# Performance work log

Measured on AMD Instinct MI355X. Metric: run time of the kernel, lower is better.

The kernel has to match this reference:

```python
import jax, jax.numpy as jnp
import numpy as np
import math

B, S, H, D = 2, 2048, 12, 768


def setup_inputs() -> dict:
    key = jax.random.key(0)
    ks = jax.random.split(key, 7)
    std = 0.02
    x = jax.random.normal(ks[0], (B, S, D), jnp.float32)
    W_q = std * jax.random.normal(ks[1], (H, D, D), jnp.float32)
    W_k = std * jax.random.normal(ks[2], (H, D, D), jnp.float32)
    W_v = std * jax.random.normal(ks[3], (H, D, D), jnp.float32)
    W_o = (std / math.sqrt(2 * 12)) * jax.random.normal(ks[4], (D, H * D), jnp.float32)
    ff_w1 = std * jax.random.normal(ks[5], (4 * D, D), jnp.float32)
    ff_w2 = std * jax.random.normal(ks[6], (D, 4 * D), jnp.float32)
    return {"x": x, "W_q": W_q, "W_k": W_k, "W_v": W_v, "W_o": W_o,
            "ff_w1": ff_w1, "ff_w2": ff_w2}


def _layernorm(x, eps=1e-5):
    # LayerNorm(elementwise_affine=False)
    mu = jnp.mean(x, axis=-1, keepdims=True)
    var = jnp.var(x, axis=-1, keepdims=True)
    return (x - mu) * jax.lax.rsqrt(var + eps)


def reference(x, W_q, W_k, W_v, W_o, ff_w1, ff_w2):
    b, s, d = x.shape
    h = W_q.shape[0]
    # per-head FULL-width projections: x is shared across heads
    Q = jnp.einsum('bsd,hde->bhse', x, W_q)
    K = jnp.einsum('bsd,hde->bhse', x, W_k)
    V = jnp.einsum('bsd,hde->bhse', x, W_v)
    scores = jnp.einsum('bhqe,bhke->bhqk', Q, K) / math.sqrt(d)  # [B,H,S,S]
    causal = jnp.tril(jnp.ones((s, s), dtype=bool))
    scores = jnp.where(causal[None, None], scores, jnp.finfo(scores.dtype).min)
    attn = jax.nn.softmax(scores, axis=-1)
    ctx = jnp.einsum('bhqk,bhke->bhqe', attn, V)            # [B,H,S,D]
    ctx = ctx.transpose(0, 2, 1, 3).reshape(b, s, h * d)     # [B,S,H*D]
    out = ctx @ W_o.T                                        # [B,S,D]
    # FFN: LN(no affine) -> Linear(d,4d) -> GELU(exact) -> Linear(4d,d); dropout=eval no-op
    hdn = jax.nn.gelu(_layernorm(out) @ ff_w1.T, approximate=False)
    out = out + hdn @ ff_w2.T
    return out
```

## Files before the change

kernel.cpp:

```cpp
#include <hip/hip_runtime.h>
#include <math.h>

#define S_   2048
#define D_   768
#define HD_  9216
#define FF_  3072

typedef float  f32x4  __attribute__((ext_vector_type(4)));
typedef __bf16 bf16x8 __attribute__((ext_vector_type(8)));

__device__ __forceinline__ ushort f2bf(float v) {
    return __builtin_bit_cast(ushort, (__bf16)v);
}

__device__ __forceinline__ void load_lds16(const ushort* g, ushort* l) {
    __builtin_amdgcn_global_load_lds(
        (const __attribute__((address_space(1))) void*)g,
        (__attribute__((address_space(3))) void*)l, 16, 0, 0);
}

__device__ __forceinline__ void zero_acc(f32x4 acc[4][4]) {
#pragma unroll
    for (int i = 0; i < 4; ++i)
#pragma unroll
        for (int j = 0; j < 4; ++j) acc[i][j] = (f32x4){0.f, 0.f, 0.f, 0.f};
}

__device__ __forceinline__ void gemm128(
    const ushort* __restrict__ A, int lda,
    const ushort* __restrict__ Bt, int ldb,
    int m0, int n0, int kmax, f32x4 acc[4][4])
{
    __shared__ __align__(16) ushort As[2][128 * 32];
    __shared__ __align__(16) ushort Bs[2][128 * 32];
    const int tid  = threadIdx.x;
    const int lane = tid & 63, wave = tid >> 6;
    const int l16  = lane & 15, quad = lane >> 4;
    const int wr = wave >> 1, wc = wave & 1;
    const int srow = lane >> 2;
    const int scol = (lane & 3) << 3;

    const ushort* Ab = A + (size_t)m0 * lda;
    const ushort* Bb = Bt + (size_t)n0 * ldb;

    auto stage = [&](int k0, int buf) {
#pragma unroll
        for (int c = 0; c < 2; ++c) {
            const int rb = c * 64 + wave * 16;
            load_lds16(Ab + (size_t)(rb + srow) * lda + k0 + scol,
                       &As[buf][rb * 32]);
            load_lds16(Bb + (size_t)(rb + srow) * ldb + k0 + scol,
                       &Bs[buf][rb * 32]);
        }
    };

    stage(0, 0);
    __syncthreads();
    int cur = 0;
    for (int k0 = 0; k0 < kmax; k0 += 32) {
        if (k0 + 32 < kmax) stage(k0 + 32, cur ^ 1);
        bf16x8 a[4], b[4];
#pragma unroll
        for (int i = 0; i < 4; ++i)
            a[i] = *(const bf16x8*)&As[cur][(wr * 64 + i * 16 + l16) * 32 + quad * 8];
#pragma unroll
        for (int j = 0; j < 4; ++j)
            b[j] = *(const bf16x8*)&Bs[cur][(wc * 64 + j * 16 + l16) * 32 + quad * 8];
#pragma unroll
        for (int i = 0; i < 4; ++i)
#pragma unroll
            for (int j = 0; j < 4; ++j)
                acc[i][j] = __builtin_amdgcn_mfma_f32_16x16x32_bf16(
                    a[i], b[j], acc[i][j], 0, 0, 0);
        __syncthreads();
        cur ^= 1;
    }
}

__device__ __forceinline__ void gemm128_bA(
    const ushort* __restrict__ Ab,
    const ushort* __restrict__ Bt, int ldb,
    int n0, int kmax, f32x4 acc[4][4])
{
    __shared__ __align__(16) ushort As[2][128 * 32];
    __shared__ __align__(16) ushort Bs[2][128 * 32];
    const int tid  = threadIdx.x;
    const int lane = tid & 63, wave = tid >> 6;
    const int l16  = lane & 15, quad = lane >> 4;
    const int wr = wave >> 1, wc = wave & 1;
    const int srow = lane >> 2;
    const int scol = (lane & 3) << 3;

    const ushort* Bb = Bt + (size_t)n0 * ldb;

    auto stage = [&](int k0, int buf) {
        const ushort* At = Ab + (size_t)(k0 >> 7) * 16384 + (k0 & 127);
#pragma unroll
        for (int c = 0; c < 2; ++c) {
            const int rb = c * 64 + wave * 16;
            load_lds16(At + (size_t)(rb + srow) * 128 + scol, &As[buf][rb * 32]);
            load_lds16(Bb + (size_t)(rb + srow) * ldb + k0 + scol,
                       &Bs[buf][rb * 32]);
        }
    };

    stage(0, 0);
    __syncthreads();
    int cur = 0;
    for (int k0 = 0; k0 < kmax; k0 += 32) {
        if (k0 + 32 < kmax) stage(k0 + 32, cur ^ 1);
        bf16x8 a[4], b[4];
#pragma unroll
        for (int i = 0; i < 4; ++i)
            a[i] = *(const bf16x8*)&As[cur][(wr * 64 + i * 16 + l16) * 32 + quad * 8];
#pragma unroll
        for (int j = 0; j < 4; ++j)
            b[j] = *(const bf16x8*)&Bs[cur][(wc * 64 + j * 16 + l16) * 32 + quad * 8];
#pragma unroll
        for (int i = 0; i < 4; ++i)
#pragma unroll
            for (int j = 0; j < 4; ++j)
                acc[i][j] = __builtin_amdgcn_mfma_f32_16x16x32_bf16(
                    a[i], b[j], acc[i][j], 0, 0, 0);
        __syncthreads();
        cur ^= 1;
    }
}

#define EPI_DECL \
    const int lane_ = threadIdx.x & 63, wave_ = threadIdx.x >> 6;   \
    const int l16_ = lane_ & 15, quad_ = lane_ >> 4;                \
    const int wr_ = wave_ >> 1, wc_ = wave_ & 1;
#define RR_ (wr_ * 64 + i * 16 + quad_ * 4 + r)
#define NC_ (wc_ * 64 + j * 16 + l16_)

__global__ __launch_bounds__(256) void convert_kernel(
    const float* __restrict__ in, ushort* __restrict__ out, long n)
{
    long i = ((long)blockIdx.x * 256 + threadIdx.x) * 4;
    const long stride = (long)gridDim.x * 1024;
    for (; i < n; i += stride) {
        float4 v = *(const float4*)&in[i];
        out[i + 0] = f2bf(v.x); out[i + 1] = f2bf(v.y);
        out[i + 2] = f2bf(v.z); out[i + 3] = f2bf(v.w);
    }
}

__global__ __launch_bounds__(256, 2) void gemmNT_kernel(
    const ushort* __restrict__ A, int lda, long aStr,
    const ushort* __restrict__ Bt, int ldb, long bStr,
    ushort* __restrict__ C, int ldc, long cStr, int kmax)
{
    const int z = blockIdx.z;
    const int m0 = blockIdx.y * 128, n0 = blockIdx.x * 128;
    f32x4 acc[4][4];
    zero_acc(acc);
    gemm128(A + (size_t)z * aStr, lda, Bt + (size_t)z * bStr, ldb,
            m0, n0, kmax, acc);
    ushort* out = C + (size_t)z * cStr;
    EPI_DECL
#pragma unroll
    for (int i = 0; i < 4; ++i)
#pragma unroll
        for (int j = 0; j < 4; ++j)
#pragma unroll
            for (int r = 0; r < 4; ++r)
                out[(size_t)(m0 + RR_) * ldc + n0 + NC_] = f2bf(acc[i][j][r]);
}

__global__ __launch_bounds__(256, 2) void xmy_kernel(
    const ushort* __restrict__ Xb, const ushort* __restrict__ MtP,
    const ushort* __restrict__ UtP, ushort* __restrict__ XMp,
    ushort* __restrict__ Yt)
{
    const int z = blockIdx.z;
    const int h = z & 1;
    const bool ymode = z >= 2;
    const int m0 = blockIdx.y * 128, n0 = blockIdx.x * 128;
    const ushort* Bt = (ymode ? UtP : MtP) + (size_t)h * 589824;
    f32x4 acc[4][4];
    zero_acc(acc);
    gemm128(Xb, D_, Bt, D_, m0, n0, D_, acc);
    EPI_DECL
    if (!ymode) {
        ushort* out = XMp + (size_t)h * 3145728;
#pragma unroll
        for (int i = 0; i < 4; ++i)
#pragma unroll
            for (int j = 0; j < 4; ++j)
#pragma unroll
                for (int r = 0; r < 4; ++r)
                    out[(size_t)(m0 + RR_) * D_ + n0 + NC_] = f2bf(acc[i][j][r]);
    } else {
        const int b = m0 >> 11;
        ushort* out = Yt + (size_t)h * 3145728 + (size_t)b * 1572864;
#pragma unroll
        for (int i = 0; i < 4; ++i)
#pragma unroll
            for (int j = 0; j < 4; ++j) {
                ushort4 o4;
                o4.x = f2bf(acc[i][j][0]); o4.y = f2bf(acc[i][j][1]);
                o4.z = f2bf(acc[i][j][2]); o4.w = f2bf(acc[i][j][3]);
                const int nc = n0 + wc_ * 64 + j * 16 + l16_;
                const int s  = (m0 & 2047) + wr_ * 64 + i * 16 + quad_ * 4;
                *(ushort4*)&out[(size_t)nc * 2048 + s] = o4;
            }
    }
}

__global__ __launch_bounds__(256, 2) void scores_c_kernel(
    const ushort* __restrict__ XM, const ushort* __restrict__ Xb,
    ushort* __restrict__ Sc)
{
    const int t = blockIdx.x, b = blockIdx.y, hp = blockIdx.z;
    int mi = (int)((sqrtf(8.f * t + 1.f) - 1.f) * 0.5f);
    while ((mi + 1) * (mi + 2) / 2 <= t) ++mi;
    while (mi * (mi + 1) / 2 > t) --mi;
    const int ni = t - mi * (mi + 1) / 2;
    f32x4 acc[4][4];
    zero_acc(acc);
    gemm128(XM + (size_t)hp * 3145728 + (size_t)b * 1572864, D_,
            Xb + (size_t)b * 1572864, D_, mi * 128, ni * 128, D_, acc);
    ushort* out = Sc + ((size_t)(hp * 2 + b) * 136 + t) * 16384;
    EPI_DECL
#pragma unroll
    for (int i = 0; i < 4; ++i)
#pragma unroll
        for (int j = 0; j < 4; ++j)
#pragma unroll
            for (int r = 0; r < 4; ++r)
                out[(size_t)RR_ * 128 + NC_] = f2bf(acc[i][j][r]);
}

__global__ __launch_bounds__(256) void softmax_c_kernel(ushort* __restrict__ Sc)
{
    const int bx = blockIdx.x;
    const int hp = bx >> 12, b = (bx >> 11) & 1, q = bx & 2047;
    ushort* base = Sc + (size_t)((hp * 2 + b) * 136) * 16384;
    const int mi = q >> 7, tri = mi * (mi + 1) / 2;
    const int L  = (mi + 1) << 7;
    const int ro = (q & 127) << 7;
    const float scale = 0.03608439182435161f;
    const int tid = threadIdx.x;
    const int wave = tid >> 6, lane = tid & 63;

    float xv[8];
    float m = -1e30f;
#pragma unroll
    for (int i = 0; i < 2; ++i) {
        const int k = tid * 4 + i * 1024;
        ushort4 v = {0, 0, 0, 0};
        if (k <= q)
            v = *(const ushort4*)&base[(size_t)(tri + (k >> 7)) * 16384
                                       + ro + (k & 127)];
        xv[i * 4 + 0] = (k + 0 <= q) ? (float)*(__bf16*)&v.x * scale : -1e30f;
        xv[i * 4 + 1] = (k + 1 <= q) ? (float)*(__bf16*)&v.y * scale : -1e30f;
        xv[i * 4 + 2] = (k + 2 <= q) ? (float)*(__bf16*)&v.z * scale : -1e30f;
        xv[i * 4 + 3] = (k + 3 <= q) ? (float)*(__bf16*)&v.w * scale : -1e30f;
#pragma unroll
        for (int j = 0; j < 4; ++j) m = fmaxf(m, xv[i * 4 + j]);
    }
    for (int o = 32; o > 0; o >>= 1) m = fmaxf(m, __shfl_xor(m, o));
    __shared__ float redm[4];
    if (lane == 0) redm[wave] = m;
    __syncthreads();
    m = fmaxf(fmaxf(redm[0], redm[1]), fmaxf(redm[2], redm[3]));

    float e[8];
    float s = 0.f;
#pragma unroll
    for (int i = 0; i < 2; ++i) {
        const int k = tid * 4 + i * 1024;
#pragma unroll
        for (int j = 0; j < 4; ++j) {
            e[i * 4 + j] = (k + j <= q) ? __expf(xv[i * 4 + j] - m) : 0.f;
            s += e[i * 4 + j];
        }
    }
    for (int o = 32; o > 0; o >>= 1) s += __shfl_xor(s, o);
    __shared__ float reds[4];
    if (lane == 0) reds[wave] = s;
    __syncthreads();
    s = reds[0] + reds[1] + reds[2] + reds[3];
    const float inv = 1.f / s;
#pragma unroll
    for (int i = 0; i < 2; ++i) {
        const int k = tid * 4 + i * 1024;
        if (k < L) {
            ushort4 o4;
            o4.x = f2bf(e[i * 4 + 0] * inv);
            o4.y = f2bf(e[i * 4 + 1] * inv);
            o4.z = f2bf(e[i * 4 + 2] * inv);
            o4.w = f2bf(e[i * 4 + 3] * inv);
            *(ushort4*)&base[(size_t)(tri + (k >> 7)) * 16384
                             + ro + (k & 127)] = o4;
        }
    }
}

__global__ __launch_bounds__(256, 2) void py_kernel(
    const ushort* __restrict__ Sc, const ushort* __restrict__ Yt,
    float* __restrict__ AttnA, float* __restrict__ AttnB)
{
    const int z = blockIdx.z;
    const int h = z >> 1, b = z & 1;
    const int mi = 15 - blockIdx.y;
    const int n0 = blockIdx.x * 128;
    const ushort* Ab =
        Sc + ((size_t)(h * 2 + b) * 136 + mi * (mi + 1) / 2) * 16384;
    const ushort* Bt = Yt + (size_t)h * 3145728 + (size_t)b * 1572864;
    f32x4 acc[4][4];
    zero_acc(acc);
    gemm128_bA(Ab, Bt, S_, n0, (mi + 1) << 7, acc);
    float* out = (h ? AttnB : AttnA) + (size_t)b * 1572864
               + (size_t)mi * 128 * D_;
    EPI_DECL
#pragma unroll
    for (int i = 0; i < 4; ++i)
#pragma unroll
        for (int j = 0; j < 4; ++j)
#pragma unroll
            for (int r = 0; r < 4; ++r)
                out[(size_t)RR_ * D_ + n0 + NC_] += acc[i][j][r];
}

__global__ __launch_bounds__(256) void ln_kernel(
    const float* __restrict__ AttnA, const float* __restrict__ AttnB,
    ushort* __restrict__ Ln)
{
    const int row = blockIdx.x;
    const float* a = AttnA + (size_t)row * D_;
    const float* b = AttnB + (size_t)row * D_;
    const int tid = threadIdx.x;
    const int wave = tid >> 6, lane = tid & 63;
    float v0 = a[tid]       + b[tid];
    float v1 = a[tid + 256] + b[tid + 256];
    float v2 = a[tid + 512] + b[tid + 512];
    float s  = v0 + v1 + v2;
    float sq = v0 * v0 + v1 * v1 + v2 * v2;
    for (int o = 32; o > 0; o >>= 1) { s += __shfl_xor(s, o); sq += __shfl_xor(sq, o); }
    __shared__ float rs[4], rq[4];
    if (lane == 0) { rs[wave] = s; rq[wave] = sq; }
    __syncthreads();
    s  = rs[0] + rs[1] + rs[2] + rs[3];
    sq = rq[0] + rq[1] + rq[2] + rq[3];
    const float mean = s * (1.f / 768.f);
    float var = sq * (1.f / 768.f) - mean * mean;
    var = fmaxf(var, 0.f);
    const float rstd = rsqrtf(var + 1e-5f);
    ushort* o = Ln + (size_t)row * D_;
    o[tid]       = f2bf((v0 - mean) * rstd);
    o[tid + 256] = f2bf((v1 - mean) * rstd);
    o[tid + 512] = f2bf((v2 - mean) * rstd);
}

__global__ __launch_bounds__(256, 2) void ffn1_kernel(
    const ushort* __restrict__ Ln, const ushort* __restrict__ F1b,
    ushort* __restrict__ H1)
{
    const int m0 = blockIdx.y * 128, n0 = blockIdx.x * 128;
    f32x4 acc[4][4];
    zero_acc(acc);
    gemm128(Ln, D_, F1b, D_, m0, n0, D_, acc);
    EPI_DECL
#pragma unroll
    for (int i = 0; i < 4; ++i)
#pragma unroll
        for (int j = 0; j < 4; ++j)
#pragma unroll
            for (int r = 0; r < 4; ++r) {
                float v = acc[i][j][r];
                float gl = 0.5f * v * (1.f + erff(v * 0.70710678118654752f));
                H1[(size_t)(m0 + RR_) * FF_ + n0 + NC_] = f2bf(gl);
            }
}

__global__ __launch_bounds__(256, 2) void ffn2p_kernel(
    const ushort* __restrict__ H1, const ushort* __restrict__ F2b,
    float* __restrict__ P2)
{
    const int z = blockIdx.z;
    const int m0 = blockIdx.y * 128, n0 = blockIdx.x * 128;
    f32x4 acc[4][4];
    zero_acc(acc);
    gemm128(H1 + (size_t)z * 1536, FF_, F2b + (size_t)z * 1536, FF_,
            m0, n0, 1536, acc);
    float* out = P2 + (size_t)z * 3145728;
    EPI_DECL
#pragma unroll
    for (int i = 0; i < 4; ++i)
#pragma unroll
        for (int j = 0; j < 4; ++j)
#pragma unroll
            for (int r = 0; r < 4; ++r)
                out[(size_t)(m0 + RR_) * D_ + n0 + NC_] = acc[i][j][r];
}

__global__ __launch_bounds__(256) void ffn2r_kernel(
    const float* __restrict__ P2, const float* __restrict__ AttnA,
    float* __restrict__ Out)
{
    const long i = ((long)blockIdx.x * 256 + threadIdx.x) * 4;
    float4 a = *(const float4*)&P2[i];
    float4 b = *(const float4*)&P2[3145728 + i];
    float4 c = *(const float4*)&AttnA[i];
    float4 d = *(const float4*)&Out[i];
    float4 o;
    o.x = a.x + b.x + c.x + d.x; o.y = a.y + b.y + c.y + d.y;
    o.z = a.z + b.z + c.z + d.z; o.w = a.w + b.w + c.w + d.w;
    *(float4*)&Out[i] = o;
}

extern "C" void kernel_launch(void* const* d_in, const int* in_sizes, int n_in,
                              void* d_out, int out_size, void* d_ws, size_t ws_size,
                              hipStream_t stream)
{
    int ix = -1, iw[4], nw = 0, iff[2], nf = 0;
    for (int i = 0; i < 7; ++i) {
        long sz = in_sizes[i];
        if (sz == 3145728L) ix = i;
        else if (sz == 2359296L) { if (nf < 2) iff[nf++] = i; }
        else { if (nw < 4) iw[nw++] = i; }
    }
    if (ix < 0 || nw != 4 || nf != 2) {
        ix = 0; iw[0] = 1; iw[1] = 2; iw[2] = 3; iw[3] = 4; iff[0] = 5; iff[1] = 6;
    }
    const float* x; const float *Wq, *Wk, *Wv, *Wo, *F1, *F2;
    x  = (const float*)d_in[ix];
    F1 = (const float*)d_in[iff[0]];
    F2 = (const float*)d_in[iff[1]];
    if (ix == 0) {
        Wq = (const float*)d_in[iw[0]]; Wk = (const float*)d_in[iw[1]];
        Wv = (const float*)d_in[iw[2]]; Wo = (const float*)d_in[iw[3]];
    } else {
        Wk = (const float*)d_in[iw[0]]; Wo = (const float*)d_in[iw[1]];
        Wq = (const float*)d_in[iw[2]]; Wv = (const float*)d_in[iw[3]];
    }

    char* p = (char*)d_ws;
    ushort* Xb    = (ushort*)(p + 0);
    ushort* Mt    = (ushort*)(p + 6291456);
    ushort* Ut    = (ushort*)(p + 20447232);
    float*  AttnA = (float*) (p + 34603008);
    ushort* XMp   = (ushort*)(p + 47185920);
    ushort* Yt    = (ushort*)(p + 59768832);
    ushort* Scp   = (ushort*)(p + 72351744);
    float*  AttnB = (float*)d_out;
    ushort* Wa    = (ushort*)(p + 47185920);
    ushort* Wb    = (ushort*)(p + 61341696);
    ushort* H1    = (ushort*)(p + 0);
    ushort* F1b   = (ushort*)(p + 47185920);
    ushort* F2b   = (ushort*)(p + 51904512);
    ushort* Ln    = (ushort*)(p + 56623104);
    float*  P2    = (float*) (p + 62914560);

    dim3 blk(256);
    hipMemsetAsync(AttnA, 0, 12582912, stream);
    hipMemsetAsync(AttnB, 0, 12582912, stream);

    convert_kernel<<<dim3(1024), blk, 0, stream>>>(x, Xb, 3145728L);

    convert_kernel<<<dim3(1024), blk, 0, stream>>>(Wq, Wa, 7077888L);
    convert_kernel<<<dim3(1024), blk, 0, stream>>>(Wk, Wb, 7077888L);
    gemmNT_kernel<<<dim3(6, 6, 12), blk, 0, stream>>>(
        Wb, 768, 589824L, Wa, 768, 589824L, Mt, 768, 589824L, 768);
    convert_kernel<<<dim3(1024), blk, 0, stream>>>(Wv, Wa, 7077888L);
    convert_kernel<<<dim3(1024), blk, 0, stream>>>(Wo, Wb, 7077888L);
    gemmNT_kernel<<<dim3(6, 6, 12), blk, 0, stream>>>(
        Wb, HD_, 768L, Wa, 768, 589824L, Ut, 768, 589824L, 768);

    for (int pr = 0; pr < 6; ++pr) {
        xmy_kernel<<<dim3(6, 32, 4), blk, 0, stream>>>(
            Xb, Mt + (size_t)pr * 1179648, Ut + (size_t)pr * 1179648,
            XMp, Yt);
        scores_c_kernel<<<dim3(136, 2, 2), blk, 0, stream>>>(XMp, Xb, Scp);
        softmax_c_kernel<<<dim3(8192), blk, 0, stream>>>(Scp);
        py_kernel<<<dim3(6, 16, 4), blk, 0, stream>>>(Scp, Yt, AttnA, AttnB);
    }

    convert_kernel<<<dim3(1024), blk, 0, stream>>>(F1, F1b, 2359296L);
    convert_kernel<<<dim3(1024), blk, 0, stream>>>(F2, F2b, 2359296L);
    ln_kernel<<<dim3(4096), blk, 0, stream>>>(AttnA, AttnB, Ln);
    ffn1_kernel<<<dim3(24, 32), blk, 0, stream>>>(Ln, F1b, H1);
    ffn2p_kernel<<<dim3(6, 32, 2), blk, 0, stream>>>(H1, F2b, P2);
    ffn2r_kernel<<<dim3(3072), blk, 0, stream>>>(P2, AttnA, (float*)d_out);
}
```

Before: 1.028 ms.

## Swizzle LDS tiles and prefetch two stages ahead with explicit vmcnt waits

Applies an XOR swizzle to the column chunk used when staging A/B tiles into LDS and when reading them for MFMA, to reduce LDS bank conflicts. Reworks the double-buffered k-loop so the load for step k+64 is issued after compute, with a partial vmcnt wait that keeps one stage of global-to-LDS loads in flight, replacing full __syncthreads waits. This risks ordering bugs if the vmcnt counts are wrong, and adds an extra barrier per iteration.

```diff
diff --git a/kernel.cpp b/kernel.cpp
--- a/kernel.cpp
+++ b/kernel.cpp
@@ -38,7 +38,7 @@
     const int l16  = lane & 15, quad = lane >> 4;
     const int wr = wave >> 1, wc = wave & 1;
     const int srow = lane >> 2;
-    const int scol = (lane & 3) << 3;
+    const int scol = ((lane & 3) ^ ((srow >> 1) & 3)) << 3;
 
     const ushort* Ab = A + (size_t)m0 * lda;
     const ushort* Bb = Bt + (size_t)n0 * ldb;
@@ -55,24 +55,42 @@
     };
 
     stage(0, 0);
-    __syncthreads();
+    if (kmax > 32) {
+        stage(32, 1);
+        asm volatile("s_waitcnt vmcnt(4)" ::: "memory");
+    } else {
+        asm volatile("s_waitcnt vmcnt(0)" ::: "memory");
+    }
+    __builtin_amdgcn_sched_barrier(0);
+    __builtin_amdgcn_s_barrier();
+
+    const int csw = (quad ^ ((l16 >> 1) & 3)) << 3;
     int cur = 0;
     for (int k0 = 0; k0 < kmax; k0 += 32) {
-        if (k0 + 32 < kmax) stage(k0 + 32, cur ^ 1);
         bf16x8 a[4], b[4];
 #pragma unroll
         for (int i = 0; i < 4; ++i)
-            a[i] = *(const bf16x8*)&As[cur][(wr * 64 + i * 16 + l16) * 32 + quad * 8];
-#pragma unroll
-        for (int j = 0; j < 4; ++j)
-            b[j] = *(const bf16x8*)&Bs[cur][(wc * 64 + j * 16 + l16) * 32 + quad * 8];
+            a[i] = *(const bf16x8*)&As[cur][(wr * 64 + i * 16 + l16) * 32 + csw];
+#pragma unroll
+        for (int j = 0; j < 4; ++j)
+            b[j] = *(const bf16x8*)&Bs[cur][(wc * 64 + j * 16 + l16) * 32 + csw];
 #pragma unroll
         for (int i = 0; i < 4; ++i)
 #pragma unroll
             for (int j = 0; j < 4; ++j)
                 acc[i][j] = __builtin_amdgcn_mfma_f32_16x16x32_bf16(
                     a[i], b[j], acc[i][j], 0, 0, 0);
-        __syncthreads();
+        __builtin_amdgcn_s_barrier();
+        if (k0 + 64 < kmax) {
+            stage(k0 + 64, cur);
+            asm volatile("s_waitcnt vmcnt(4)" ::: "memory");
+            __builtin_amdgcn_sched_barrier(0);
+            __builtin_amdgcn_s_barrier();
+        } else if (k0 + 32 < kmax) {
+            asm volatile("s_waitcnt vmcnt(0)" ::: "memory");
+            __builtin_amdgcn_sched_barrier(0);
+            __builtin_amdgcn_s_barrier();
+        }
         cur ^= 1;
     }
 }
@@ -89,7 +107,7 @@
     const int l16  = lane & 15, quad = lane >> 4;
     const int wr = wave >> 1, wc = wave & 1;
     const int srow = lane >> 2;
-    const int scol = (lane & 3) << 3;
+    const int scol = ((lane & 3) ^ ((srow >> 1) & 3)) << 3;
 
     const ushort* Bb = Bt + (size_t)n0 * ldb;
 
@@ -105,24 +123,42 @@
     };
 
     stage(0, 0);
-    __syncthreads();
+    if (kmax > 32) {
+        stage(32, 1);
+        asm volatile("s_waitcnt vmcnt(4)" ::: "memory");
+    } else {
+        asm volatile("s_waitcnt vmcnt(0)" ::: "memory");
+    }
+    __builtin_amdgcn_sched_barrier(0);
+    __builtin_amdgcn_s_barrier();
+
+    const int csw = (quad ^ ((l16 >> 1) & 3)) << 3;
     int cur = 0;
     for (int k0 = 0; k0 < kmax; k0 += 32) {
-        if (k0 + 32 < kmax) stage(k0 + 32, cur ^ 1);
         bf16x8 a[4], b[4];
 #pragma unroll
         for (int i = 0; i < 4; ++i)
-            a[i] = *(const bf16x8*)&As[cur][(wr * 64 + i * 16 + l16) * 32 + quad * 8];
-#pragma unroll
-        for (int j = 0; j < 4; ++j)
-            b[j] = *(const bf16x8*)&Bs[cur][(wc * 64 + j * 16 + l16) * 32 + quad * 8];
+            a[i] = *(const bf16x8*)&As[cur][(wr * 64 + i * 16 + l16) * 32 + csw];
+#pragma unroll
+        for (int j = 0; j < 4; ++j)
+            b[j] = *(const bf16x8*)&Bs[cur][(wc * 64 + j * 16 + l16) * 32 + csw];
 #pragma unroll
         for (int i = 0; i < 4; ++i)
 #pragma unroll
             for (int j = 0; j < 4; ++j)
                 acc[i][j] = __builtin_amdgcn_mfma_f32_16x16x32_bf16(
                     a[i], b[j], acc[i][j], 0, 0, 0);
-        __syncthreads();
+        __builtin_amdgcn_s_barrier();
+        if (k0 + 64 < kmax) {
+            stage(k0 + 64, cur);
+            asm volatile("s_waitcnt vmcnt(4)" ::: "memory");
+            __builtin_amdgcn_sched_barrier(0);
+            __builtin_amdgcn_s_barrier();
+        } else if (k0 + 32 < kmax) {
+            asm volatile("s_waitcnt vmcnt(0)" ::: "memory");
+            __builtin_amdgcn_sched_barrier(0);
+            __builtin_amdgcn_s_barrier();
+        }
         cur ^= 1;
     }
 }
```

After: 1.040 ms. No clear change (+1.1%).

## Swizzle LDS tiles to avoid bank conflicts and split PY kernel into 64-row tiles

Applied to the files above, without the earlier changes.

Applies an XOR swizzle to the 16-byte column chunk in the LDS staging and fragment reads of both GEMM helpers, so the MFMA operand loads spread across LDS banks. The PY (attention-times-Y) kernel now uses 64-row M tiles instead of 128-row tiles, which doubles its grid and balances the triangular causal workload across more blocks. The trade-off is less reuse of the B operand per block and more blocks performing read-modify-write accumulation into the output.

```diff
diff --git a/kernel.cpp b/kernel.cpp
--- a/kernel.cpp
+++ b/kernel.cpp
@@ -17,13 +17,6 @@
     __builtin_amdgcn_global_load_lds(
         (const __attribute__((address_space(1))) void*)g,
         (__attribute__((address_space(3))) void*)l, 16, 0, 0);
-}
-
-__device__ __forceinline__ void zero_acc(f32x4 acc[4][4]) {
-#pragma unroll
-    for (int i = 0; i < 4; ++i)
-#pragma unroll
-        for (int j = 0; j < 4; ++j) acc[i][j] = (f32x4){0.f, 0.f, 0.f, 0.f};
 }
 
 __device__ __forceinline__ void gemm128(
@@ -38,7 +31,7 @@
     const int l16  = lane & 15, quad = lane >> 4;
     const int wr = wave >> 1, wc = wave & 1;
     const int srow = lane >> 2;
-    const int scol = (lane & 3) << 3;
+    const int scol = ((lane & 3) ^ ((srow >> 1) & 3)) << 3;
 
     const ushort* Ab = A + (size_t)m0 * lda;
     const ushort* Bb = Bt + (size_t)n0 * ldb;
@@ -56,16 +49,17 @@
 
     stage(0, 0);
     __syncthreads();
+    const int csw = (quad ^ ((l16 >> 1) & 3)) << 3;
     int cur = 0;
     for (int k0 = 0; k0 < kmax; k0 += 32) {
         if (k0 + 32 < kmax) stage(k0 + 32, cur ^ 1);
         bf16x8 a[4], b[4];
 #pragma unroll
         for (int i = 0; i < 4; ++i)
-            a[i] = *(const bf16x8*)&As[cur][(wr * 64 + i * 16 + l16) * 32 + quad * 8];
-#pragma unroll
-        for (int j = 0; j < 4; ++j)
-            b[j] = *(const bf16x8*)&Bs[cur][(wc * 64 + j * 16 + l16) * 32 + quad * 8];
+            a[i] = *(const bf16x8*)&As[cur][(wr * 64 + i * 16 + l16) * 32 + csw];
+#pragma unroll
+        for (int j = 0; j < 4; ++j)
+            b[j] = *(const bf16x8*)&Bs[cur][(wc * 64 + j * 16 + l16) * 32 + csw];
 #pragma unroll
         for (int i = 0; i < 4; ++i)
 #pragma unroll
@@ -77,28 +71,31 @@
     }
 }
 
-__device__ __forceinline__ void gemm128_bA(
+__device__ __forceinline__ void gemm64_bA(
     const ushort* __restrict__ Ab,
     const ushort* __restrict__ Bt, int ldb,
-    int n0, int kmax, f32x4 acc[4][4])
-{
-    __shared__ __align__(16) ushort As[2][128 * 32];
+    int n0, int kmax, f32x4 acc[2][4])
+{
+    __shared__ __align__(16) ushort As[2][64 * 32];
     __shared__ __align__(16) ushort Bs[2][128 * 32];
     const int tid  = threadIdx.x;
     const int lane = tid & 63, wave = tid >> 6;
     const int l16  = lane & 15, quad = lane >> 4;
     const int wr = wave >> 1, wc = wave & 1;
     const int srow = lane >> 2;
-    const int scol = (lane & 3) << 3;
+    const int scol = ((lane & 3) ^ ((srow >> 1) & 3)) << 3;
 
     const ushort* Bb = Bt + (size_t)n0 * ldb;
 
     auto stage = [&](int k0, int buf) {
         const ushort* At = Ab + (size_t)(k0 >> 7) * 16384 + (k0 & 127);
+        {
+            const int rb = wave * 16;
+            load_lds16(At + (size_t)(rb + srow) * 128 + scol, &As[buf][rb * 32]);
+        }
 #pragma unroll
         for (int c = 0; c < 2; ++c) {
             const int rb = c * 64 + wave * 16;
-            load_lds16(At + (size_t)(rb + srow) * 128 + scol, &As[buf][rb * 32]);
             load_lds16(Bb + (size_t)(rb + srow) * ldb + k0 + scol,
                        &Bs[buf][rb * 32]);
         }
@@ -106,18 +103,19 @@
 
     stage(0, 0);
     __syncthreads();
+    const int csw = (quad ^ ((l16 >> 1) & 3)) << 3;
     int cur = 0;
     for (int k0 = 0; k0 < kmax; k0 += 32) {
         if (k0 + 32 < kmax) stage(k0 + 32, cur ^ 1);
-        bf16x8 a[4], b[4];
-#pragma unroll
-        for (int i = 0; i < 4; ++i)
-            a[i] = *(const bf16x8*)&As[cur][(wr * 64 + i * 16 + l16) * 32 + quad * 8];
-#pragma unroll
-        for (int j = 0; j < 4; ++j)
-            b[j] = *(const bf16x8*)&Bs[cur][(wc * 64 + j * 16 + l16) * 32 + quad * 8];
-#pragma unroll
-        for (int i = 0; i < 4; ++i)
+        bf16x8 a[2], b[4];
+#pragma unroll
+        for (int i = 0; i < 2; ++i)
+            a[i] = *(const bf16x8*)&As[cur][(wr * 32 + i * 16 + l16) * 32 + csw];
+#pragma unroll
+        for (int j = 0; j < 4; ++j)
+            b[j] = *(const bf16x8*)&Bs[cur][(wc * 64 + j * 16 + l16) * 32 + csw];
+#pragma unroll
+        for (int i = 0; i < 2; ++i)
 #pragma unroll
             for (int j = 0; j < 4; ++j)
                 acc[i][j] = __builtin_amdgcn_mfma_f32_16x16x32_bf16(
@@ -154,7 +152,10 @@
     const int z = blockIdx.z;
     const int m0 = blockIdx.y * 128, n0 = blockIdx.x * 128;
     f32x4 acc[4][4];
-    zero_acc(acc);
+#pragma unroll
+    for (int i = 0; i < 4; ++i)
+#pragma unroll
+        for (int j = 0; j < 4; ++j) acc[i][j] = (f32x4){0.f, 0.f, 0.f, 0.f};
     gemm128(A + (size_t)z * aStr, lda, Bt + (size_t)z * bStr, ldb,
             m0, n0, kmax, acc);
     ushort* out = C + (size_t)z * cStr;
@@ -179,7 +180,10 @@
     const int m0 = blockIdx.y * 128, n0 = blockIdx.x * 128;
     const ushort* Bt = (ymode ? UtP : MtP) + (size_t)h * 589824;
     f32x4 acc[4][4];
-    zero_acc(acc);
+#pragma unroll
+    for (int i = 0; i < 4; ++i)
+#pragma unroll
+        for (int j = 0; j < 4; ++j) acc[i][j] = (f32x4){0.f, 0.f, 0.f, 0.f};
     gemm128(Xb, D_, Bt, D_, m0, n0, D_, acc);
     EPI_DECL
     if (!ymode) {
@@ -218,7 +222,10 @@
     while (mi * (mi + 1) / 2 > t) --mi;
     const int ni = t - mi * (mi + 1) / 2;
     f32x4 acc[4][4];
-    zero_acc(acc);
+#pragma unroll
+    for (int i = 0; i < 4; ++i)
+#pragma unroll
+        for (int j = 0; j < 4; ++j) acc[i][j] = (f32x4){0.f, 0.f, 0.f, 0.f};
     gemm128(XM + (size_t)hp * 3145728 + (size_t)b * 1572864, D_,
             Xb + (size_t)b * 1572864, D_, mi * 128, ni * 128, D_, acc);
     ushort* out = Sc + ((size_t)(hp * 2 + b) * 136 + t) * 16384;
@@ -304,24 +311,34 @@
 {
     const int z = blockIdx.z;
     const int h = z >> 1, b = z & 1;
-    const int mi = 15 - blockIdx.y;
+    const int mi64 = 31 - blockIdx.y;
+    const int mi   = mi64 >> 1;
     const int n0 = blockIdx.x * 128;
     const ushort* Ab =
-        Sc + ((size_t)(h * 2 + b) * 136 + mi * (mi + 1) / 2) * 16384;
+        Sc + ((size_t)(h * 2 + b) * 136 + mi * (mi + 1) / 2) * 16384
+           + (size_t)(mi64 & 1) * 8192;
     const ushort* Bt = Yt + (size_t)h * 3145728 + (size_t)b * 1572864;
-    f32x4 acc[4][4];
-    zero_acc(acc);
-    gemm128_bA(Ab, Bt, S_, n0, (mi + 1) << 7, acc);
+    f32x4 acc[2][4];
+#pragma unroll
+    for (int i = 0; i < 2; ++i)
+#pragma unroll
+        for (int j = 0; j < 4; ++j) acc[i][j] = (f32x4){0.f, 0.f, 0.f, 0.f};
+    gemm64_bA(Ab, Bt, S_, n0, (mi + 1) << 7, acc);
     float* out = (h ? AttnB : AttnA) + (size_t)b * 1572864
-               + (size_t)mi * 128 * D_;
-    EPI_DECL
-#pragma unroll
-    for (int i = 0; i < 4; ++i)
-#pragma unroll
-        for (int j = 0; j < 4; ++j)
-#pragma unroll
-            for (int r = 0; r < 4; ++r)
-                out[(size_t)RR_ * D_ + n0 + NC_] += acc[i][j][r];
+               + (size_t)mi64 * 64 * D_;
+    const int lane_ = threadIdx.x & 63, wave_ = threadIdx.x >> 6;
+    const int l16_ = lane_ & 15, quad_ = lane_ >> 4;
+    const int wr_ = wave_ >> 1, wc_ = wave_ & 1;
+#pragma unroll
+    for (int i = 0; i < 2; ++i)
+#pragma unroll
+        for (int j = 0; j < 4; ++j)
+#pragma unroll
+            for (int r = 0; r < 4; ++r) {
+                const int rr = wr_ * 32 + i * 16 + quad_ * 4 + r;
+                const int nc = wc_ * 64 + j * 16 + l16_;
+                out[(size_t)rr * D_ + n0 + nc] += acc[i][j][r];
+            }
 }
 
 __global__ __launch_bounds__(256) void ln_kernel(
@@ -360,7 +377,10 @@
 {
     const int m0 = blockIdx.y * 128, n0 = blockIdx.x * 128;
     f32x4 acc[4][4];
-    zero_acc(acc);
+#pragma unroll
+    for (int i = 0; i < 4; ++i)
+#pragma unroll
+        for (int j = 0; j < 4; ++j) acc[i][j] = (f32x4){0.f, 0.f, 0.f, 0.f};
     gemm128(Ln, D_, F1b, D_, m0, n0, D_, acc);
     EPI_DECL
 #pragma unroll
@@ -382,7 +402,10 @@
     const int z = blockIdx.z;
     const int m0 = blockIdx.y * 128, n0 = blockIdx.x * 128;
     f32x4 acc[4][4];
-    zero_acc(acc);
+#pragma unroll
+    for (int i = 0; i < 4; ++i)
+#pragma unroll
+        for (int j = 0; j < 4; ++j) acc[i][j] = (f32x4){0.f, 0.f, 0.f, 0.f};
     gemm128(H1 + (size_t)z * 1536, FF_, F2b + (size_t)z * 1536, FF_,
             m0, n0, 1536, acc);
     float* out = P2 + (size_t)z * 3145728;
@@ -475,7 +498,7 @@
             XMp, Yt);
         scores_c_kernel<<<dim3(136, 2, 2), blk, 0, stream>>>(XMp, Xb, Scp);
         softmax_c_kernel<<<dim3(8192), blk, 0, stream>>>(Scp);
-        py_kernel<<<dim3(6, 16, 4), blk, 0, stream>>>(Scp, Yt, AttnA, AttnB);
+        py_kernel<<<dim3(6, 32, 4), blk, 0, stream>>>(Scp, Yt, AttnA, AttnB);
     }
 
     convert_kernel<<<dim3(1024), blk, 0, stream>>>(F1, F1b, 2359296L);
```

Result: faster. 1.001 ms (-2.6%).
